# Optimization experiments

Measured on AMD Instinct MI355X. Metric: run time of the kernel, lower is better.

## Reference

```python
import jax, jax.numpy as jnp
import numpy as np

DIM, HID, E, K = 1024, 2048, 8, 2


def setup_inputs() -> dict:
    key = jax.random.key(0)
    ks = jax.random.split(key, 5)
    x = jax.random.normal(ks[0], (2, 2048, DIM), dtype=jnp.float32)
    # router (torch zero-inits; use small random so routing is non-degenerate)
    router_w = jax.random.normal(ks[1], (DIM, E), dtype=jnp.float32) * 0.02
    router_b = jnp.zeros((E,), dtype=jnp.float32)
    # stacked expert params: w12 [E, dim, 2*hidden], w3 [E, hidden, dim]
    w12 = jax.random.normal(ks[2], (E, DIM, 2 * HID), dtype=jnp.float32) * 0.02
    w3 = jax.random.normal(ks[3], (E, HID, DIM), dtype=jnp.float32) * 0.02
    return {"x": x, "router_w": router_w, "router_b": router_b, "w12": w12, "w3": w3}


def reference(x, router_w, router_b, w12, w3):
    # router logits [b, s, e]; eval mode -> no jitter noise
    logits = jnp.einsum("bsd,de->bse", x, router_w) + router_b
    scores = jax.nn.sigmoid(logits)
    top_v, top_i = jax.lax.top_k(scores, K)            # [b, s, k]
    rw = top_v / (jnp.sum(top_v, axis=-1, keepdims=True) + 1e-6)
    # per-token combine weight for each expert (0 if not routed)
    oh = jax.nn.one_hot(top_i, E, dtype=x.dtype)       # [b, s, k, e]
    cw = jnp.einsum("bsk,bske->bse", rw, oh)           # [b, s, e]
    # dense all-expert SwiGLU (matches original masked-dense math)
    x12 = jnp.einsum("bsd,edh->bseh", x, w12)          # [b, s, e, 2H]
    x1, x2 = jnp.split(x12, 2, axis=-1)
    h = jax.nn.silu(x1) * x2                           # [b, s, e, H]
    eout = jnp.einsum("bseh,ehd->bsed", h, w3)         # [b, s, e, dim]
    out = jnp.einsum("bsed,bse->bsd", eout, cw)
    aux_loss = 0.01 * jnp.mean(logits ** 2)
    return out, aux_loss
```

## Files before the change

### kernel.cpp

```cpp
#include <hip/hip_runtime.h>
#include <hip/hip_bf16.h>
#include <stdint.h>

typedef __bf16 bf16_t;
typedef __bf16 bf16x8 __attribute__((ext_vector_type(8)));
typedef __bf16 bf16x4 __attribute__((ext_vector_type(4)));
typedef float f32x4 __attribute__((ext_vector_type(4)));

#define T_TOK 4096
#define DIM   1024
#define HID   2048
#define NE    8
#define MAXT  72

__device__ __forceinline__ void gload_lds16(const void* g, void* l) {
  __builtin_amdgcn_global_load_lds(
      (const __attribute__((address_space(1))) unsigned int*)g,
      (__attribute__((address_space(3))) unsigned int*)l, 16, 0, 0);
}

__global__ __launch_bounds__(256) void k_wt(const float* __restrict__ in,
                                            bf16_t* __restrict__ out,
                                            int K, int N) {
  __shared__ float tile[64][65];
  const size_t eoff = (size_t)blockIdx.z * K * N;
  const int k0 = blockIdx.y * 64, n0 = blockIdx.x * 64;
  const int tid = threadIdx.x;
#pragma unroll
  for (int it = 0; it < 4; ++it) {
    int k = (tid >> 4) + it * 16;
    int n = (tid & 15) * 4;
    float4 v = *(const float4*)(in + eoff + (size_t)(k0 + k) * N + n0 + n);
    tile[k][n] = v.x; tile[k][n + 1] = v.y; tile[k][n + 2] = v.z; tile[k][n + 3] = v.w;
  }
  __syncthreads();
#pragma unroll
  for (int it = 0; it < 2; ++it) {
    int n = (tid >> 3) + it * 32;
    int kc = (tid & 7) * 8;
    bf16x8 o;
#pragma unroll
    for (int j = 0; j < 8; ++j) o[j] = (bf16_t)tile[kc + j][n];
    *(bf16x8*)(out + eoff + (size_t)(n0 + n) * K + k0 + kc) = o;
  }
}

__global__ __launch_bounds__(256) void k_router(const float* __restrict__ x,
    const float* __restrict__ rw, const float* __restrict__ rb,
    int* __restrict__ counts, int* __restrict__ top_i, float* __restrict__ top_w,
    float* __restrict__ aux, bf16_t* __restrict__ xb) {
  int t = blockIdx.x * 4 + (threadIdx.x >> 6);
  int lane = threadIdx.x & 63;
  const float* xt = x + (size_t)t * DIM;
  float acc[8] = {0.f,0.f,0.f,0.f,0.f,0.f,0.f,0.f};
#pragma unroll
  for (int it = 0; it < 4; ++it) {
    int i = (it * 64 + lane) * 4;
    float4 xv = *(const float4*)(xt + i);
    bf16x4 o;
    o[0] = (bf16_t)xv.x; o[1] = (bf16_t)xv.y; o[2] = (bf16_t)xv.z; o[3] = (bf16_t)xv.w;
    *(bf16x4*)(xb + (size_t)t * DIM + i) = o;
#pragma unroll
    for (int c = 0; c < 4; ++c) {
      float v = (c == 0) ? xv.x : (c == 1) ? xv.y : (c == 2) ? xv.z : xv.w;
      float4 r0 = *(const float4*)(rw + (size_t)(i + c) * 8);
      float4 r1 = *(const float4*)(rw + (size_t)(i + c) * 8 + 4);
      acc[0] += v * r0.x; acc[1] += v * r0.y; acc[2] += v * r0.z; acc[3] += v * r0.w;
      acc[4] += v * r1.x; acc[5] += v * r1.y; acc[6] += v * r1.z; acc[7] += v * r1.w;
    }
  }
#pragma unroll
  for (int m = 32; m >= 1; m >>= 1) {
#pragma unroll
    for (int e = 0; e < 8; ++e) acc[e] += __shfl_xor(acc[e], m, 64);
  }
  if (lane == 0) {
    float s[8]; float sumsq = 0.f;
#pragma unroll
    for (int e = 0; e < 8; ++e) {
      float lg = acc[e] + rb[e];
      sumsq += lg * lg;
      s[e] = 1.f / (1.f + __expf(-lg));
    }
    int i1 = 0;
#pragma unroll
    for (int e = 1; e < 8; ++e) if (s[e] > s[i1]) i1 = e;
    int i2 = (i1 == 0) ? 1 : 0;
#pragma unroll
    for (int e = 0; e < 8; ++e) if (e != i1 && s[e] > s[i2]) i2 = e;
    float v1 = s[i1], v2 = s[i2];
    float den = v1 + v2 + 1e-6f;
    top_i[2 * t]     = i1; top_i[2 * t + 1] = i2;
    top_w[2 * t]     = v1 / den;
    top_w[2 * t + 1] = v2 / den;
    atomicAdd(&counts[i1], 1);
    atomicAdd(&counts[i2], 1);
    atomicAdd(aux, 0.01f * sumsq * (1.f / 32768.f));
  }
}

__global__ void k_plan(const int* __restrict__ counts, int* __restrict__ base,
                       int* __restrict__ tile_e, int* __restrict__ tile_m0) {
  if (threadIdx.x == 0) {
    int s = 0, nt = 0;
    for (int e = 0; e < NE; ++e) {
      base[e] = s;
      int c = counts[e];
      for (int m0 = 0; m0 < c; m0 += 128) { tile_e[nt] = e; tile_m0[nt] = m0; ++nt; }
      s += c;
    }
    for (; nt < MAXT; ++nt) tile_e[nt] = -1;
  }
}

__global__ __launch_bounds__(256) void k_gather(const int* __restrict__ top_i,
    const float* __restrict__ top_w, const int* __restrict__ base,
    int* __restrict__ fill, int* __restrict__ slot_token, float* __restrict__ slot_wt,
    int* __restrict__ slot_of) {
  int t = blockIdx.x * 256 + threadIdx.x;
  if (t >= T_TOK) return;
#pragma unroll
  for (int j = 0; j < 2; ++j) {
    int e = top_i[2 * t + j];
    int p = atomicAdd(&fill[e], 1);
    int g = base[e] + p;
    slot_token[g] = t;
    slot_wt[g]    = top_w[2 * t + j];
    slot_of[2 * t + j] = g;
  }
}

__global__ __launch_bounds__(256) void k_gemm1(
    const bf16_t* __restrict__ xb, const bf16_t* __restrict__ w12t,
    const int* __restrict__ counts, const int* __restrict__ base,
    const int* __restrict__ tile_e, const int* __restrict__ tile_m0,
    const int* __restrict__ slot_token, bf16_t* __restrict__ h) {
  const int e = tile_e[blockIdx.y];
  if (e < 0) return;
  const int m0  = tile_m0[blockIdx.y];
  const int cnt = counts[e];
  const int bas = base[e];
  const int n0 = blockIdx.x * 64;
  const bf16_t* W1 = w12t + (size_t)e * (4096u * 1024u) + (size_t)n0 * 1024u;
  const bf16_t* W2 = W1 + (size_t)2048 * 1024;

  __shared__ bf16_t sA[128 * 64];
  __shared__ bf16_t sB1[64 * 64];
  __shared__ bf16_t sB2[64 * 64];

  const int tid = threadIdx.x, lane = tid & 63, wid = tid >> 6;
  const int wr = wid >> 1, wc = wid & 1;
  const int lr = lane >> 3, sw = (lane & 7) ^ lr;

  int tokA[4];
#pragma unroll
  for (int i = 0; i < 4; ++i) {
    int row = m0 + wid * 32 + i * 8 + lr;
    tokA[i] = slot_token[bas + (row < cnt ? row : cnt - 1)];
  }

  f32x4 acc1[4][2] = {};
  f32x4 acc2[4][2] = {};

  for (int k0 = 0; k0 < DIM; k0 += 64) {
#pragma unroll
    for (int i = 0; i < 4; ++i)
      gload_lds16(xb + (size_t)tokA[i] * DIM + k0 + sw * 8,
                  sA + (wid * 32 + i * 8) * 64);
#pragma unroll
    for (int i = 0; i < 2; ++i) {
      int n = wid * 16 + i * 8 + lr;
      gload_lds16(W1 + (size_t)n * 1024 + k0 + sw * 8, sB1 + (wid * 16 + i * 8) * 64);
      gload_lds16(W2 + (size_t)n * 1024 + k0 + sw * 8, sB2 + (wid * 16 + i * 8) * 64);
    }
    __syncthreads();
#pragma unroll
    for (int kk = 0; kk < 2; ++kk) {
      const int g = kk * 4 + (lane >> 4);
      bf16x8 a[4], b1[2], b2[2];
#pragma unroll
      for (int mf = 0; mf < 4; ++mf) {
        int r = wr * 64 + mf * 16 + (lane & 15);
        a[mf] = *(const bf16x8*)(sA + r * 64 + ((g ^ (r & 7)) << 3));
      }
#pragma unroll
      for (int nf = 0; nf < 2; ++nf) {
        int n = wc * 32 + nf * 16 + (lane & 15);
        b1[nf] = *(const bf16x8*)(sB1 + n * 64 + ((g ^ (n & 7)) << 3));
        b2[nf] = *(const bf16x8*)(sB2 + n * 64 + ((g ^ (n & 7)) << 3));
      }
#pragma unroll
      for (int mf = 0; mf < 4; ++mf)
#pragma unroll
        for (int nf = 0; nf < 2; ++nf) {
          acc1[mf][nf] = __builtin_amdgcn_mfma_f32_16x16x32_bf16(a[mf], b1[nf], acc1[mf][nf], 0, 0, 0);
          acc2[mf][nf] = __builtin_amdgcn_mfma_f32_16x16x32_bf16(a[mf], b2[nf], acc2[mf][nf], 0, 0, 0);
        }
    }
    __syncthreads();
  }
#pragma unroll
  for (int mf = 0; mf < 4; ++mf)
#pragma unroll
    for (int r = 0; r < 4; ++r) {
      int m = wr * 64 + mf * 16 + ((lane >> 4) << 2) + r;
      if (m0 + m < cnt) {
        size_t rowoff = (size_t)(bas + m0 + m) * HID + n0;
#pragma unroll
        for (int nf = 0; nf < 2; ++nf) {
          int col = wc * 32 + nf * 16 + (lane & 15);
          float d1 = acc1[mf][nf][r], d2 = acc2[mf][nf][r];
          h[rowoff + col] = (bf16_t)((d1 / (1.f + __expf(-d1))) * d2);
        }
      }
    }
}

__global__ __launch_bounds__(256) void k_gemm2(
    const bf16_t* __restrict__ h, const bf16_t* __restrict__ w3t,
    const int* __restrict__ counts, const int* __restrict__ base,
    const int* __restrict__ tile_e, const int* __restrict__ tile_m0,
    const float* __restrict__ slot_wt, bf16_t* __restrict__ eout) {
  const int e = tile_e[blockIdx.y];
  if (e < 0) return;
  const int m0  = tile_m0[blockIdx.y];
  const int cnt = counts[e];
  const int bas = base[e];
  const int n0 = blockIdx.x * 128;
  const bf16_t* W = w3t + (size_t)e * (1024u * 2048u);

  __shared__ bf16_t sA[128 * 64];
  __shared__ bf16_t sB[128 * 64];

  const int tid = threadIdx.x, lane = tid & 63, wid = tid >> 6;
  const int wr = wid >> 1, wc = wid & 1;
  const int lr = lane >> 3, sw = (lane & 7) ^ lr;

  int rowA[4];
#pragma unroll
  for (int i = 0; i < 4; ++i) {
    int row = m0 + wid * 32 + i * 8 + lr;
    rowA[i] = bas + (row < cnt ? row : cnt - 1);
  }

  f32x4 acc[4][4] = {};

  for (int k0 = 0; k0 < HID; k0 += 64) {
#pragma unroll
    for (int i = 0; i < 4; ++i) {
      gload_lds16(h + (size_t)rowA[i] * HID + k0 + sw * 8,
                  sA + (wid * 32 + i * 8) * 64);
      int n = wid * 32 + i * 8 + lr;
      gload_lds16(W + (size_t)(n0 + n) * 2048 + k0 + sw * 8,
                  sB + (wid * 32 + i * 8) * 64);
    }
    __syncthreads();
#pragma unroll
    for (int kk = 0; kk < 2; ++kk) {
      const int g = kk * 4 + (lane >> 4);
      bf16x8 a[4], b[4];
#pragma unroll
      for (int mf = 0; mf < 4; ++mf) {
        int r = wr * 64 + mf * 16 + (lane & 15);
        a[mf] = *(const bf16x8*)(sA + r * 64 + ((g ^ (r & 7)) << 3));
      }
#pragma unroll
      for (int nf = 0; nf < 4; ++nf) {
        int n = wc * 64 + nf * 16 + (lane & 15);
        b[nf] = *(const bf16x8*)(sB + n * 64 + ((g ^ (n & 7)) << 3));
      }
#pragma unroll
      for (int mf = 0; mf < 4; ++mf)
#pragma unroll
        for (int nf = 0; nf < 4; ++nf)
          acc[mf][nf] = __builtin_amdgcn_mfma_f32_16x16x32_bf16(a[mf], b[nf], acc[mf][nf], 0, 0, 0);
    }
    __syncthreads();
  }
#pragma unroll
  for (int mf = 0; mf < 4; ++mf)
#pragma unroll
    for (int r = 0; r < 4; ++r) {
      int m = wr * 64 + mf * 16 + ((lane >> 4) << 2) + r;
      if (m0 + m < cnt) {
        int gs = bas + m0 + m;
        float wt = slot_wt[gs];
        size_t o = (size_t)gs * DIM + n0;
#pragma unroll
        for (int nf = 0; nf < 4; ++nf) {
          int col = wc * 64 + nf * 16 + (lane & 15);
          eout[o + col] = (bf16_t)(acc[mf][nf][r] * wt);
        }
      }
    }
}

__global__ __launch_bounds__(256) void k_combine(const bf16_t* __restrict__ eout,
    const int* __restrict__ slot_of, float* __restrict__ out) {
  const int t = blockIdx.x;
  const int c = threadIdx.x * 4;
  const int g0 = slot_of[2 * t], g1 = slot_of[2 * t + 1];
  bf16x4 a = *(const bf16x4*)(eout + (size_t)g0 * DIM + c);
  bf16x4 b = *(const bf16x4*)(eout + (size_t)g1 * DIM + c);
  float4 o;
  o.x = (float)a[0] + (float)b[0];
  o.y = (float)a[1] + (float)b[1];
  o.z = (float)a[2] + (float)b[2];
  o.w = (float)a[3] + (float)b[3];
  *(float4*)(out + (size_t)t * DIM + c) = o;
}

extern "C" void kernel_launch(void* const* d_in, const int* in_sizes, int n_in,
                              void* d_out, int out_size, void* d_ws, size_t ws_size,
                              hipStream_t stream) {
  const float* x   = (const float*)d_in[0];
  const float* rw  = (const float*)d_in[1];
  const float* rb  = (const float*)d_in[2];
  const float* w12 = (const float*)d_in[3];
  const float* w3  = (const float*)d_in[4];
  float* out = (float*)d_out;
  float* aux = out + (size_t)T_TOK * DIM;

  char* ws = (char*)d_ws;
  int*   counts     = (int*)(ws + 0);
  int*   fill       = (int*)(ws + 64);
  int*   base       = (int*)(ws + 128);
  int*   top_i      = (int*)(ws + 4096);
  float* top_w      = (float*)(ws + 4096 + 32768);
  int*   slot_token = (int*)(ws + 4096 + 65536);
  float* slot_wt    = (float*)(ws + 4096 + 98304);
  int*   slot_of    = (int*)(ws + 4096 + 131072);
  int*   tile_e     = (int*)(ws + 4096 + 163840);
  int*   tile_m0    = (int*)(ws + 4096 + 164352);
  bf16_t* xb        = (bf16_t*)(ws + 262144);
  bf16_t* h         = (bf16_t*)(ws + 262144 + 8388608);
  bf16_t* wT        = (bf16_t*)(ws + 262144 + 8388608 + 33554432);
  bf16_t* eout      = (bf16_t*)((char*)wT + 33554432);

  hipMemsetAsync(ws, 0, 256, stream);
  hipMemsetAsync(aux, 0, sizeof(float), stream);

  k_wt<<<dim3(64, 16, NE), dim3(256), 0, stream>>>(w12, wT, DIM, 2 * HID);
  k_router<<<dim3(T_TOK / 4), dim3(256), 0, stream>>>(x, rw, rb, counts, top_i, top_w,
                                                      aux, xb);
  k_plan<<<dim3(1), dim3(64), 0, stream>>>(counts, base, tile_e, tile_m0);
  k_gather<<<dim3(T_TOK / 256), dim3(256), 0, stream>>>(top_i, top_w, base, fill,
                                                        slot_token, slot_wt, slot_of);
  k_gemm1<<<dim3(HID / 64, MAXT), dim3(256), 0, stream>>>(
      xb, wT, counts, base, tile_e, tile_m0, slot_token, h);
  k_wt<<<dim3(16, 32, NE), dim3(256), 0, stream>>>(w3, wT, HID, DIM);
  k_gemm2<<<dim3(DIM / 128, MAXT), dim3(256), 0, stream>>>(
      h, wT, counts, base, tile_e, tile_m0, slot_wt, eout);
  k_combine<<<dim3(T_TOK), dim3(256), 0, stream>>>(eout, slot_of, out);
}
```

Measured before the change: 399.3 us.

## Double-buffer LDS tiles in both expert GEMMs with async prefetch

Both grouped GEMM kernels now use two LDS buffers and issue global-to-LDS loads two k-steps ahead. Explicit vmcnt waits and raw barriers replace the per-iteration __syncthreads. The aim is to hide global load latency behind MFMA work instead of stalling each iteration. LDS use doubles (64KB in gemm2), which may cut occupancy, and the hand-written vmcnt(8) counts must match the number of loads each stage issues.

```diff
diff --git a/kernel.cpp b/kernel.cpp
--- a/kernel.cpp
+++ b/kernel.cpp
@@ -144,9 +144,9 @@
   const bf16_t* W1 = w12t + (size_t)e * (4096u * 1024u) + (size_t)n0 * 1024u;
   const bf16_t* W2 = W1 + (size_t)2048 * 1024;
 
-  __shared__ bf16_t sA[128 * 64];
-  __shared__ bf16_t sB1[64 * 64];
-  __shared__ bf16_t sB2[64 * 64];
+  __shared__ bf16_t sA[2][128 * 64];
+  __shared__ bf16_t sB1[2][64 * 64];
+  __shared__ bf16_t sB2[2][64 * 64];
 
   const int tid = threadIdx.x, lane = tid & 63, wid = tid >> 6;
   const int wr = wid >> 1, wc = wid & 1;
@@ -159,21 +159,32 @@
     tokA[i] = slot_token[bas + (row < cnt ? row : cnt - 1)];
   }
 
+  auto stage = [&](int p, int k0) {
+#pragma unroll
+    for (int i = 0; i < 4; ++i)
+      gload_lds16(xb + (size_t)tokA[i] * DIM + k0 + sw * 8,
+                  &sA[p][(wid * 32 + i * 8) * 64]);
+#pragma unroll
+    for (int i = 0; i < 2; ++i) {
+      int n = wid * 16 + i * 8 + lr;
+      gload_lds16(W1 + (size_t)n * 1024 + k0 + sw * 8, &sB1[p][(wid * 16 + i * 8) * 64]);
+      gload_lds16(W2 + (size_t)n * 1024 + k0 + sw * 8, &sB2[p][(wid * 16 + i * 8) * 64]);
+    }
+  };
+
   f32x4 acc1[4][2] = {};
   f32x4 acc2[4][2] = {};
 
-  for (int k0 = 0; k0 < DIM; k0 += 64) {
-#pragma unroll
-    for (int i = 0; i < 4; ++i)
-      gload_lds16(xb + (size_t)tokA[i] * DIM + k0 + sw * 8,
-                  sA + (wid * 32 + i * 8) * 64);
-#pragma unroll
-    for (int i = 0; i < 2; ++i) {
-      int n = wid * 16 + i * 8 + lr;
-      gload_lds16(W1 + (size_t)n * 1024 + k0 + sw * 8, sB1 + (wid * 16 + i * 8) * 64);
-      gload_lds16(W2 + (size_t)n * 1024 + k0 + sw * 8, sB2 + (wid * 16 + i * 8) * 64);
-    }
-    __syncthreads();
+  stage(0, 0);
+  stage(1, 64);
+
+  const int NT = DIM / 64;
+  for (int t = 0; t < NT; ++t) {
+    const int p = t & 1;
+    if (t + 2 < NT) asm volatile("s_waitcnt vmcnt(8)" ::: "memory");
+    else            asm volatile("s_waitcnt vmcnt(0)" ::: "memory");
+    __builtin_amdgcn_s_barrier();
+    asm volatile("" ::: "memory");
 #pragma unroll
     for (int kk = 0; kk < 2; ++kk) {
       const int g = kk * 4 + (lane >> 4);
@@ -181,13 +192,13 @@
 #pragma unroll
       for (int mf = 0; mf < 4; ++mf) {
         int r = wr * 64 + mf * 16 + (lane & 15);
-        a[mf] = *(const bf16x8*)(sA + r * 64 + ((g ^ (r & 7)) << 3));
+        a[mf] = *(const bf16x8*)(&sA[p][r * 64 + ((g ^ (r & 7)) << 3)]);
       }
 #pragma unroll
       for (int nf = 0; nf < 2; ++nf) {
         int n = wc * 32 + nf * 16 + (lane & 15);
-        b1[nf] = *(const bf16x8*)(sB1 + n * 64 + ((g ^ (n & 7)) << 3));
-        b2[nf] = *(const bf16x8*)(sB2 + n * 64 + ((g ^ (n & 7)) << 3));
+        b1[nf] = *(const bf16x8*)(&sB1[p][n * 64 + ((g ^ (n & 7)) << 3)]);
+        b2[nf] = *(const bf16x8*)(&sB2[p][n * 64 + ((g ^ (n & 7)) << 3)]);
       }
 #pragma unroll
       for (int mf = 0; mf < 4; ++mf)
@@ -197,8 +208,12 @@
           acc2[mf][nf] = __builtin_amdgcn_mfma_f32_16x16x32_bf16(a[mf], b2[nf], acc2[mf][nf], 0, 0, 0);
         }
     }
-    __syncthreads();
-  }
+    __builtin_amdgcn_sched_barrier(0);
+    __builtin_amdgcn_s_barrier();
+    asm volatile("" ::: "memory");
+    if (t + 2 < NT) stage(p, (t + 2) * 64);
+  }
+
 #pragma unroll
   for (int mf = 0; mf < 4; ++mf)
 #pragma unroll
@@ -229,8 +244,8 @@
   const int n0 = blockIdx.x * 128;
   const bf16_t* W = w3t + (size_t)e * (1024u * 2048u);
 
-  __shared__ bf16_t sA[128 * 64];
-  __shared__ bf16_t sB[128 * 64];
+  __shared__ bf16_t sA[2][128 * 64];
+  __shared__ bf16_t sB[2][128 * 64];
 
   const int tid = threadIdx.x, lane = tid & 63, wid = tid >> 6;
   const int wr = wid >> 1, wc = wid & 1;
@@ -243,18 +258,27 @@
     rowA[i] = bas + (row < cnt ? row : cnt - 1);
   }
 
+  auto stage = [&](int p, int k0) {
+#pragma unroll
+    for (int i = 0; i < 4; ++i) {
+      int rr = wid * 32 + i * 8;
+      gload_lds16(h + (size_t)rowA[i] * HID + k0 + sw * 8, &sA[p][rr * 64]);
+      gload_lds16(W + (size_t)(n0 + rr + lr) * 2048 + k0 + sw * 8, &sB[p][rr * 64]);
+    }
+  };
+
   f32x4 acc[4][4] = {};
 
-  for (int k0 = 0; k0 < HID; k0 += 64) {
-#pragma unroll
-    for (int i = 0; i < 4; ++i) {
-      gload_lds16(h + (size_t)rowA[i] * HID + k0 + sw * 8,
-                  sA + (wid * 32 + i * 8) * 64);
-      int n = wid * 32 + i * 8 + lr;
-      gload_lds16(W + (size_t)(n0 + n) * 2048 + k0 + sw * 8,
-                  sB + (wid * 32 + i * 8) * 64);
-    }
-    __syncthreads();
+  stage(0, 0);
+  stage(1, 64);
+
+  const int NT = HID / 64;
+  for (int t = 0; t < NT; ++t) {
+    const int p = t & 1;
+    if (t + 2 < NT) asm volatile("s_waitcnt vmcnt(8)" ::: "memory");
+    else            asm volatile("s_waitcnt vmcnt(0)" ::: "memory");
+    __builtin_amdgcn_s_barrier();
+    asm volatile("" ::: "memory");
 #pragma unroll
     for (int kk = 0; kk < 2; ++kk) {
       const int g = kk * 4 + (lane >> 4);
@@ -262,12 +286,12 @@
 #pragma unroll
       for (int mf = 0; mf < 4; ++mf) {
         int r = wr * 64 + mf * 16 + (lane & 15);
-        a[mf] = *(const bf16x8*)(sA + r * 64 + ((g ^ (r & 7)) << 3));
+        a[mf] = *(const bf16x8*)(&sA[p][r * 64 + ((g ^ (r & 7)) << 3)]);
       }
 #pragma unroll
       for (int nf = 0; nf < 4; ++nf) {
         int n = wc * 64 + nf * 16 + (lane & 15);
-        b[nf] = *(const bf16x8*)(sB + n * 64 + ((g ^ (n & 7)) << 3));
+        b[nf] = *(const bf16x8*)(&sB[p][n * 64 + ((g ^ (n & 7)) << 3)]);
       }
 #pragma unroll
       for (int mf = 0; mf < 4; ++mf)
@@ -275,8 +299,12 @@
         for (int nf = 0; nf < 4; ++nf)
           acc[mf][nf] = __builtin_amdgcn_mfma_f32_16x16x32_bf16(a[mf], b[nf], acc[mf][nf], 0, 0, 0);
     }
-    __syncthreads();
-  }
+    __builtin_amdgcn_sched_barrier(0);
+    __builtin_amdgcn_s_barrier();
+    asm volatile("" ::: "memory");
+    if (t + 2 < NT) stage(p, (t + 2) * 64);
+  }
+
 #pragma unroll
   for (int mf = 0; mf < 4; ++mf)
 #pragma unroll
```

Measured after the change: 382.1 us. -4.3%, faster.
